# Performance work log

Hardware: AMD Instinct MI355X
Metric: run time of the kernel (lower is better)

## Reference

```python
import jax, jax.numpy as jnp
import numpy as np

H, Hk, Hv, Dk, Dv, K = 1536, 8, 16, 64, 64, 4
KEY_DIM = Hk * Dk            # 512
VALUE_DIM = Hv * Dv          # 1024
CONV_DIM = 2 * KEY_DIM + VALUE_DIM  # 2048


def setup_inputs() -> dict:
    key = jax.random.key(0)
    ks = jax.random.split(key, 12)
    s = 0.02
    return {
        "hidden_states": jax.random.normal(ks[0], (1, H, 1, 1), jnp.float32),
        "W_qkv": jax.random.normal(ks[1], (CONV_DIM, H), jnp.float32) * s,
        "W_z": jax.random.normal(ks[2], (VALUE_DIM, H), jnp.float32) * s,
        "W_a": jax.random.normal(ks[3], (Hv, H), jnp.float32) * s,
        "W_b": jax.random.normal(ks[4], (Hv, H), jnp.float32) * s,
        "W_out": jax.random.normal(ks[5], (H, VALUE_DIM), jnp.float32) * s,
        "conv1d_weight": jax.random.normal(ks[6], (CONV_DIM, K), jnp.float32) * 0.1,
        "A_log": jax.random.normal(ks[7], (Hv,), jnp.float32) * 0.1,
        "dt_bias": jax.random.normal(ks[8], (Hv,), jnp.float32) * 0.1,
        "norm_weight": jnp.ones((Dv,), jnp.float32),
        "state": jax.random.normal(ks[9], (1, Hv, Dk, Dv), jnp.float32) * 0.05,
        "conv_cache": jax.random.normal(ks[10], (1, CONV_DIM, K - 1), jnp.float32) * 0.1,
    }


def _l2n(t):
    # l2_normalize with eps=1e-12 (matches torch rsqrt(sum(x^2)+eps))
    return t * jax.lax.rsqrt(jnp.sum(t * t, axis=-1, keepdims=True) + 1e-12)


def reference(hidden_states, W_qkv, W_z, W_a, W_b, W_out, conv1d_weight,
              A_log, dt_bias, norm_weight, state, conv_cache):
    x = hidden_states.reshape(-1)                       # [H]
    qkv = W_qkv @ x                                     # [CONV_DIM]
    z = (W_z @ x).reshape(Hv, Dv)                       # gate, [Hv, Dv]
    a = W_a @ x                                         # [Hv]
    beta = jax.nn.sigmoid(W_b @ x)                      # [Hv]

    # causal conv as weighted sum over cache + current token
    combined = jnp.concatenate([conv_cache[0], qkv[:, None]], axis=1)  # [CONV_DIM, K]
    conv_out = jax.nn.silu(jnp.sum(combined * conv1d_weight, axis=1))  # [CONV_DIM]

    q = conv_out[:KEY_DIM].reshape(Hk, Dk)
    k = conv_out[KEY_DIM:2 * KEY_DIM].reshape(Hk, Dk)
    v = conv_out[2 * KEY_DIM:].reshape(Hv, Dv)

    rep = Hv // Hk                                      # kv_group = 2
    q = jnp.repeat(q, rep, axis=0)                      # [Hv, Dk]
    k = jnp.repeat(k, rep, axis=0)
    q = _l2n(q) * (Dk ** -0.5)
    k = _l2n(k)

    # gated decay
    g = -jnp.exp(A_log) * jax.nn.softplus(a + dt_bias)  # [Hv]
    st = state[0] * jnp.exp(g)[:, None, None]           # [Hv, Dk, Dv]

    # delta-rule update
    retrieved = jnp.einsum('hkv,hk->hv', st, k)         # [Hv, Dv]
    delta = (v - retrieved) * beta[:, None]             # [Hv, Dv]
    new_state = st + jnp.einsum('hk,hv->hkv', k, delta) # [Hv, Dk, Dv]

    out = jnp.einsum('hkv,hk->hv', new_state, q)        # [Hv, Dv]

    # gated RMSNorm over Dv
    var = jnp.mean(out * out, axis=-1, keepdims=True)
    out = norm_weight * (out * jax.lax.rsqrt(var + 1e-6)) * jax.nn.silu(z)

    y = W_out @ out.reshape(-1)                         # [H]
    return y.reshape(1, -1, 1, 1)
```

## Files before the change

### kernel.cpp

```cpp
#include <hip/hip_runtime.h>

#define H 1536
#define HK 8
#define HV 16
#define DK 64
#define DV 64
#define KEY_DIM 512
#define VALUE_DIM 1024
#define CONV_DIM 2048
#define NROWS1 (CONV_DIM + VALUE_DIM + HV + HV)
#define NBLK 776
#define NOUT_BLK 384
#define MAGIC 0x5A17ED

__device__ __forceinline__ float wave_reduce_sum(float v) {
#pragma unroll
    for (int off = 32; off > 0; off >>= 1) v += __shfl_xor(v, off, 64);
    return v;
}

__device__ __forceinline__ void st_dev(float* p, float v) {
    __hip_atomic_store(p, v, __ATOMIC_RELAXED, __HIP_MEMORY_SCOPE_AGENT);
}
__device__ __forceinline__ float ld_dev(const float* p) {
    return __hip_atomic_load(p, __ATOMIC_RELAXED, __HIP_MEMORY_SCOPE_AGENT);
}
__device__ __forceinline__ void st_flag(int* p, int v) {
    __hip_atomic_store(p, v, __ATOMIC_RELAXED, __HIP_MEMORY_SCOPE_AGENT);
}
__device__ __forceinline__ int ld_flag(const int* p) {
    return __hip_atomic_load(p, __ATOMIC_RELAXED, __HIP_MEMORY_SCOPE_AGENT);
}
__device__ __forceinline__ float2 ld_dev2(const float* p) {
    unsigned long long u = __hip_atomic_load((const unsigned long long*)p,
                                             __ATOMIC_RELAXED, __HIP_MEMORY_SCOPE_AGENT);
    union { unsigned long long u; float2 f; } c; c.u = u; return c.f;
}
template <int SLEEP>
__device__ __forceinline__ void wait_flag(const int* p) {
    while (ld_flag(p) != MAGIC) __builtin_amdgcn_s_sleep(SLEEP);
}

__global__ __launch_bounds__(256, 4) void fused_decode(
        const float* __restrict__ x,
        const float* __restrict__ Wqkv, const float* __restrict__ Wz,
        const float* __restrict__ Wa,   const float* __restrict__ Wb,
        const float* __restrict__ Wout,
        const float* __restrict__ conv_w, const float* __restrict__ conv_cache,
        const float* __restrict__ A_log, const float* __restrict__ dt_bias,
        const float* __restrict__ norm_w, const float* __restrict__ state,
        float* __restrict__ ws, float* __restrict__ og,
        int* __restrict__ flg,
        int* __restrict__ ogflg,
        float* __restrict__ y) {
    const int blk  = blockIdx.x;
    const int tid  = threadIdx.x;
    const int wave = tid >> 6;
    const int lane = tid & 63;

    __shared__ float q_s[64], k_s[64], v_s[64];
    __shared__ float red_r[256], red_o[256];
    __shared__ float scal[3];

    float4 wreg[4];
    const int orow = blk * 4 + wave;
    if (blk < NOUT_BLK) {
        const float4* w4 = (const float4*)(Wout + (size_t)orow * VALUE_DIM);
#pragma unroll
        for (int j = 0; j < 4; ++j) wreg[j] = w4[lane + 64 * j];
    }

    {
        const int row = blk * 4 + wave;
        const float* wrow;
        if (row < CONV_DIM)                       wrow = Wqkv + (size_t)row * H;
        else if (row < CONV_DIM + VALUE_DIM)      wrow = Wz + (size_t)(row - CONV_DIM) * H;
        else if (row < CONV_DIM + VALUE_DIM + HV) wrow = Wa + (size_t)(row - CONV_DIM - VALUE_DIM) * H;
        else                                      wrow = Wb + (size_t)(row - CONV_DIM - VALUE_DIM - HV) * H;
        const float4* w4 = (const float4*)wrow;
        const float4* x4 = (const float4*)x;
        float acc = 0.f;
#pragma unroll
        for (int j = 0; j < 6; ++j) {
            float4 a = w4[lane + 64 * j];
            float4 b = x4[lane + 64 * j];
            acc += a.x * b.x + a.y * b.y + a.z * b.z + a.w * b.w;
        }
        acc = wave_reduce_sum(acc);
        if (lane == 0) st_dev(&ws[row], acc);
        asm volatile("s_waitcnt vmcnt(0)" ::: "memory");
        if (lane == 0) st_flag(&flg[row], MAGIC);
    }

    if (blk >= NOUT_BLK) return;

    if (blk < HV) {
        const int h = blk;
        const int grp = wave;
        if (grp < 3) {
            int i;
            if (grp == 0)      i = (h >> 1) * 64 + lane;
            else if (grp == 1) i = KEY_DIM + (h >> 1) * 64 + lane;
            else               i = 2 * KEY_DIM + h * 64 + lane;
            wait_flag<1>(&flg[i]);
            float raw = conv_cache[i * 3 + 0] * conv_w[i * 4 + 0]
                      + conv_cache[i * 3 + 1] * conv_w[i * 4 + 1]
                      + conv_cache[i * 3 + 2] * conv_w[i * 4 + 2]
                      + ld_dev(&ws[i])        * conv_w[i * 4 + 3];
            float c = raw / (1.f + expf(-raw));
            if (grp == 2) {
                v_s[lane] = c;
            } else {
                float ss  = wave_reduce_sum(c * c);
                float inv = rsqrtf(ss + 1e-12f);
                if (grp == 0) q_s[lane] = c * inv * 0.125f;
                else          k_s[lane] = c * inv;
            }
        } else if (lane == 0) {
            const int ra = CONV_DIM + VALUE_DIM + h;
            const int rb = ra + HV;
            wait_flag<1>(&flg[ra]);
            wait_flag<1>(&flg[rb]);
            float aa = ld_dev(&ws[ra]) + dt_bias[h];
            float sp = (aa > 20.f) ? aa : log1pf(expf(aa));
            scal[0] = expf(-expf(A_log[h]) * sp);
            float braw = ld_dev(&ws[rb]);
            scal[1] = 1.f / (1.f + expf(-braw));
        }
        __syncthreads();

        const float* st = state + (size_t)h * DK * DV;
        float pr = 0.f, po = 0.f;
        const int k0 = wave * 16;
#pragma unroll
        for (int kk = 0; kk < 16; ++kk) {
            float s = st[(k0 + kk) * 64 + lane];
            pr += s * k_s[k0 + kk];
            po += s * q_s[k0 + kk];
        }
        red_r[tid] = pr;
        red_o[tid] = po;
        if (wave == 0) {
            float t = wave_reduce_sum(k_s[lane] * q_s[lane]);
            if (lane == 0) scal[2] = t;
        }
        __syncthreads();

        if (tid < 64) {
            const float decay = scal[0], beta = scal[1], kq = scal[2];
            float r = (red_r[tid] + red_r[64 + tid] + red_r[128 + tid] + red_r[192 + tid]) * decay;
            float o = (red_o[tid] + red_o[64 + tid] + red_o[128 + tid] + red_o[192 + tid]) * decay;
            float delta = (v_s[tid] - r) * beta;
            float outv  = o + delta * kq;
            float ss  = wave_reduce_sum(outv * outv);
            float inv = rsqrtf(ss * (1.f / 64.f) + 1e-6f);
            const int zr = CONV_DIM + h * 64 + tid;
            wait_flag<1>(&flg[zr]);
            float zz  = ld_dev(&ws[zr]);
            float gate = zz / (1.f + expf(-zz));
            st_dev(&og[h * 64 + tid], norm_w[tid] * outv * inv * gate);
            asm volatile("s_waitcnt vmcnt(0)" ::: "memory");
            if (tid == 0) st_flag(&ogflg[h], MAGIC);
        }
    }

    {
        if (lane < HV) wait_flag<4>(&ogflg[lane]);
        float acc = 0.f;
#pragma unroll
        for (int j = 0; j < 4; ++j) {
            const int base = (lane + 64 * j) * 4;
            float2 b0 = ld_dev2(og + base);
            float2 b1 = ld_dev2(og + base + 2);
            acc += wreg[j].x * b0.x + wreg[j].y * b0.y
                 + wreg[j].z * b1.x + wreg[j].w * b1.y;
        }
        acc = wave_reduce_sum(acc);
        if (lane == 0) y[orow] = acc;
    }
}

extern "C" void kernel_launch(void* const* d_in, const int* in_sizes, int n_in,
                              void* d_out, int out_size, void* d_ws, size_t ws_size,
                              hipStream_t stream) {
    const float* x     = (const float*)d_in[0];
    const float* Wqkv  = (const float*)d_in[1];
    const float* Wz    = (const float*)d_in[2];
    const float* Wa    = (const float*)d_in[3];
    const float* Wb    = (const float*)d_in[4];
    const float* Wout  = (const float*)d_in[5];
    const float* convw = (const float*)d_in[6];
    const float* Alog  = (const float*)d_in[7];
    const float* dtb   = (const float*)d_in[8];
    const float* normw = (const float*)d_in[9];
    const float* state = (const float*)d_in[10];
    const float* cch   = (const float*)d_in[11];

    float* ws  = (float*)d_ws;
    float* og  = (float*)((char*)d_ws + 16384);
    int*  flg  = (int*)((char*)d_ws + 32768);
    int*  ogfl = (int*)((char*)d_ws + 49152);
    float* y   = (float*)d_out;

    fused_decode<<<NBLK, 256, 0, stream>>>(
        x, Wqkv, Wz, Wa, Wb, Wout, convw, cch, Alog, dtb, normw, state,
        ws, og, flg, ogfl, y);
}
```

Baseline: 100.4 us.

## Prefetch state into registers, reorder GEMV rows, and use a single master flag

Blocks 0..15 now load their slice of the recurrent state into registers early, before the first GEMV, so the load overlaps with other work. Row assignment is permuted so the small W_a and W_b rows are computed first by the lowest blocks, letting the head blocks get decay and beta sooner. Instead of every output block polling sixteen per-head flags, block 0 waits on them and publishes one master flag that the other blocks poll. This cuts polling traffic, but adds a serial hop through block 0, raises register pressure from the 16-float state buffer, and relies on all blocks being co-resident.

Result: no change. 98.92 us (-1.4%).

```diff
diff --git a/kernel.cpp b/kernel.cpp
--- a/kernel.cpp
+++ b/kernel.cpp
@@ -52,6 +52,7 @@
         float* __restrict__ ws, float* __restrict__ og,
         int* __restrict__ flg,
         int* __restrict__ ogflg,
+        int* __restrict__ master,
         float* __restrict__ y) {
     const int blk  = blockIdx.x;
     const int tid  = threadIdx.x;
@@ -69,14 +70,25 @@
 #pragma unroll
         for (int j = 0; j < 4; ++j) wreg[j] = w4[lane + 64 * j];
     }
+    float sreg[16];
+    if (blk < HV) {
+        const float* st = state + (size_t)blk * DK * DV;
+#pragma unroll
+        for (int kk = 0; kk < 16; ++kk)
+            sreg[kk] = st[(wave * 16 + kk) * 64 + lane];
+    }
 
     {
         const int row = blk * 4 + wave;
-        const float* wrow;
-        if (row < CONV_DIM)                       wrow = Wqkv + (size_t)row * H;
-        else if (row < CONV_DIM + VALUE_DIM)      wrow = Wz + (size_t)(row - CONV_DIM) * H;
-        else if (row < CONV_DIM + VALUE_DIM + HV) wrow = Wa + (size_t)(row - CONV_DIM - VALUE_DIM) * H;
-        else                                      wrow = Wb + (size_t)(row - CONV_DIM - VALUE_DIM - HV) * H;
+        int slot; const float* wrow;
+        if (row < HV)            { slot = CONV_DIM + VALUE_DIM + row;            wrow = Wa + (size_t)row * H; }
+        else if (row < 2 * HV)   { slot = CONV_DIM + VALUE_DIM + row;            wrow = Wb + (size_t)(row - HV) * H; }
+        else {
+            const int r2 = row - 2 * HV;
+            slot = r2;
+            wrow = (r2 < CONV_DIM) ? Wqkv + (size_t)r2 * H
+                                   : Wz + (size_t)(r2 - CONV_DIM) * H;
+        }
         const float4* w4 = (const float4*)wrow;
         const float4* x4 = (const float4*)x;
         float acc = 0.f;
@@ -87,9 +99,9 @@
             acc += a.x * b.x + a.y * b.y + a.z * b.z + a.w * b.w;
         }
         acc = wave_reduce_sum(acc);
-        if (lane == 0) st_dev(&ws[row], acc);
+        if (lane == 0) st_dev(&ws[slot], acc);
         asm volatile("s_waitcnt vmcnt(0)" ::: "memory");
-        if (lane == 0) st_flag(&flg[row], MAGIC);
+        if (lane == 0) st_flag(&flg[slot], MAGIC);
     }
 
     if (blk >= NOUT_BLK) return;
@@ -129,14 +141,12 @@
         }
         __syncthreads();
 
-        const float* st = state + (size_t)h * DK * DV;
         float pr = 0.f, po = 0.f;
         const int k0 = wave * 16;
 #pragma unroll
         for (int kk = 0; kk < 16; ++kk) {
-            float s = st[(k0 + kk) * 64 + lane];
-            pr += s * k_s[k0 + kk];
-            po += s * q_s[k0 + kk];
+            pr += sreg[kk] * k_s[k0 + kk];
+            po += sreg[kk] * q_s[k0 + kk];
         }
         red_r[tid] = pr;
         red_o[tid] = po;
@@ -164,8 +174,18 @@
         }
     }
 
+    if (blk == 0) {
+        if (tid == 0) {
+#pragma unroll
+            for (int hh = 0; hh < HV; ++hh) wait_flag<1>(&ogflg[hh]);
+            st_flag(master, MAGIC);
+        }
+    } else {
+        if (tid == 0) wait_flag<2>(master);
+    }
+    __syncthreads();
+
     {
-        if (lane < HV) wait_flag<4>(&ogflg[lane]);
         float acc = 0.f;
 #pragma unroll
         for (int j = 0; j < 4; ++j) {
@@ -196,13 +216,14 @@
     const float* state = (const float*)d_in[10];
     const float* cch   = (const float*)d_in[11];
 
-    float* ws  = (float*)d_ws;
-    float* og  = (float*)((char*)d_ws + 16384);
-    int*  flg  = (int*)((char*)d_ws + 32768);
-    int*  ogfl = (int*)((char*)d_ws + 49152);
-    float* y   = (float*)d_out;
+    float* ws     = (float*)d_ws;
+    float* og     = (float*)((char*)d_ws + 16384);
+    int*  flg     = (int*)((char*)d_ws + 32768);
+    int*  ogfl    = (int*)((char*)d_ws + 49152);
+    int*  master  = (int*)((char*)d_ws + 49152 + 256);
+    float* y      = (float*)d_out;
 
     fused_decode<<<NBLK, 256, 0, stream>>>(
         x, Wqkv, Wz, Wa, Wb, Wout, convw, cch, Alog, dtb, normw, state,
-        ws, og, flg, ogfl, y);
-}
+        ws, og, flg, ogfl, master, y);
+}
```
